# Kernel optimization log

Hardware: AMD Instinct MI355X
Metric: run time of the kernel (lower is better)

## Reference

```python
import jax, jax.numpy as jnp
import numpy as np

H, D = 4, 32            # heads, per-head dim
HD = H * D              # hidden_dim = output_dim = 128
ND, NG = 10000, 30000   # num disease / gene nodes
E_DG, E_GD, E_GG = 150000, 150000, 300000
L = 2                   # num HGTConv layers


def setup_inputs() -> dict:
    key = jax.random.key(0)
    ks = jax.random.split(key, 16)
    s = 0.05
    return {
        "x_d": jax.random.normal(ks[0], (ND, HD), jnp.float32),
        "x_g": jax.random.normal(ks[1], (NG, HD), jnp.float32),
        "src_dg": jax.random.randint(ks[2], (E_DG,), 0, ND),
        "dst_dg": jax.random.randint(ks[3], (E_DG,), 0, NG),
        "src_gd": jax.random.randint(ks[4], (E_GD,), 0, NG),
        "dst_gd": jax.random.randint(ks[5], (E_GD,), 0, ND),
        "src_gg": jax.random.randint(ks[6], (E_GG,), 0, NG),
        "dst_gg": jax.random.randint(ks[7], (E_GG,), 0, NG),
        # fused K/Q/V projection per node type, stacked over layers
        "Wkqv_d": jax.random.normal(ks[8], (L, HD, 3 * HD), jnp.float32) * s,
        "bkqv_d": jnp.zeros((L, 3 * HD), jnp.float32),
        "Wkqv_g": jax.random.normal(ks[9], (L, HD, 3 * HD), jnp.float32) * s,
        "bkqv_g": jnp.zeros((L, 3 * HD), jnp.float32),
        # output linear per node type
        "Wout_d": jax.random.normal(ks[10], (L, HD, HD), jnp.float32) * s,
        "bout_d": jnp.zeros((L, HD), jnp.float32),
        "Wout_g": jax.random.normal(ks[11], (L, HD, HD), jnp.float32) * s,
        "bout_g": jnp.zeros((L, HD), jnp.float32),
        # learnable skip gates per node type
        "skip_d": jnp.ones((L,), jnp.float32),
        "skip_g": jnp.ones((L,), jnp.float32),
        # per edge-type relation matrices (key, message) and priors, 3 edge types
        "arel": jax.random.normal(ks[12], (L, 3, H, D, D), jnp.float32) * s,
        "mrel": jax.random.normal(ks[13], (L, 3, H, D, D), jnp.float32) * s,
        "prel": jnp.ones((L, 3, H), jnp.float32),
    }


def _hgt_forward(x_d, x_g, src_dg, dst_dg, src_gd, dst_gd, src_gg, dst_gg,
                 Wkqv_d, bkqv_d, Wkqv_g, bkqv_g, Wout_d, bout_d, Wout_g, bout_g,
                 skip_d, skip_g, arel, mrel, prel):
    scale = 1.0 / (D ** 0.5)
    for l in range(L):
        def kqv(x, W, b):
            t = (x @ W + b).reshape(-1, 3, H, D)
            return t[:, 0], t[:, 1], t[:, 2]

        k_d, q_d, v_d = kqv(x_d, Wkqv_d[l], bkqv_d[l])
        k_g, q_g, v_g = kqv(x_g, Wkqv_g[l], bkqv_g[l])

        def edge_msgs(k_src, v_src, q_dst, src, dst, et):
            # gather src K/V, transform by per-edge-type relation matrices
            ke = jnp.einsum('ehd,hdf->ehf', k_src[src], arel[l, et])  # [E,H,D]
            ve = jnp.einsum('ehd,hdf->ehf', v_src[src], mrel[l, et])  # [E,H,D]
            a = jnp.sum(q_dst[dst] * ke, axis=-1) * prel[l, et] * scale  # [E,H]
            return a, ve

        a_dg, v_dg = edge_msgs(k_d, v_d, q_g, src_dg, dst_dg, 0)
        a_gd, v_gd = edge_msgs(k_g, v_g, q_d, src_gd, dst_gd, 1)
        a_gg, v_gg = edge_msgs(k_g, v_g, q_g, src_gg, dst_gg, 2)

        def aggregate(alphas, vals, dsts, n):
            # segment softmax over ALL incoming edges of a dst node (across edge types)
            a = jnp.concatenate(alphas, axis=0)
            v = jnp.concatenate(vals, axis=0)
            d = jnp.concatenate(dsts, axis=0)
            amax = jax.ops.segment_max(a, d, num_segments=n)
            ex = jnp.exp(a - amax[d])
            den = jax.ops.segment_sum(ex, d, num_segments=n)
            w = ex / den[d]
            out = jax.ops.segment_sum(w[:, :, None] * v, d, num_segments=n)
            return out.reshape(n, HD)

        agg_g = aggregate([a_dg, a_gg], [v_dg, v_gg], [dst_dg, dst_gg], NG)
        agg_d = aggregate([a_gd], [v_gd], [dst_gd], ND)

        def update(agg, x, Wout, bout, skip):
            o = jax.nn.gelu(agg) @ Wout + bout
            g = jax.nn.sigmoid(skip)
            return g * o + (1.0 - g) * x

        x_d = update(agg_d, x_d, Wout_d[l], bout_d[l], skip_d[l])
        x_g = update(agg_g, x_g, Wout_g[l], bout_g[l], skip_g[l])
    return x_d, x_g


def reference(x_d, x_g, src_dg, dst_dg, src_gd, dst_gd, src_gg, dst_gg,
              Wkqv_d, bkqv_d, Wkqv_g, bkqv_g, Wout_d, bout_d, Wout_g, bout_g,
              skip_d, skip_g, arel, mrel, prel):
    return _hgt_forward(x_d, x_g, src_dg, dst_dg, src_gd, dst_gd, src_gg, dst_gg,
                        Wkqv_d, bkqv_d, Wkqv_g, bkqv_g, Wout_d, bout_d, Wout_g, bout_g,
                        skip_d, skip_g, arel, mrel, prel)
```

## Files before the change

kernel.cpp:

```cpp
#include <hip/hip_runtime.h>
#include <hip/hip_bf16.h>

#define H 4
#define D 32
#define HD 128
#define ND 10000
#define NG 30000
#define E_DG 150000
#define E_GD 150000
#define E_GG 300000
#define NE (E_DG + E_GD + E_GG)
#define EG (E_DG + E_GG)
#define NLAYER 2
#define NBG 30
#define NBD 10
#define NSCAN (NBG + NBD)
#define OCG 640
#define OCD 384
#define GOFF ((size_t)ND * OCD)
#define NSCAT 2344
#define NQUAD 625
#define XLSTRIDE 136

typedef _Float16 f16;
typedef __attribute__((ext_vector_type(2))) _Float16 f16x2;
typedef __attribute__((ext_vector_type(4))) _Float16 f16x4;
typedef __attribute__((ext_vector_type(8))) _Float16 f16x8;
typedef __attribute__((ext_vector_type(4))) float f32x4;

__device__ __forceinline__ float bu(unsigned short u) {
    return __uint_as_float(((unsigned)u) << 16);
}
__device__ __forceinline__ float ldraw(const void* p, size_t i, bool isf32) {
    return isf32 ? ((const float*)p)[i] : bu(((const unsigned short*)p)[i]);
}
__device__ __forceinline__ float gelu(float v) {
    const float c = 0.79788456080286536f * (v + 0.044715f * v * v * v);
    return 0.5f * v * (1.0f + tanhf(c));
}

__device__ __forceinline__ void combine_one(
    int idx, int GENE, bool isf32,
    const void* W, const void* bvec,
    const void* arel, const void* mrel, const void* prel,
    f16* __restrict__ Wp, float* __restrict__ bp) {
    const int OC = GENE ? OCG : OCD;
    const int l = idx / (OC * 128);
    const int rem = idx - l * OC * 128;
    const int col = rem >> 7;
    const int d = rem & 127;
    const int g = col >> 7;
    const int jj = col & 127;
    const int h = jj >> 5, f = jj & 31;
    const size_t wbase = (size_t)l * 128 * 384;
    const size_t bbase = (size_t)l * 384;
    float val, bv = 0.f;
    if (g == 0) {
        val = ldraw(W, wbase + d * 384 + 128 + jj, isf32);
        bv = ldraw(bvec, bbase + 128 + jj, isf32);
    } else {
        const int et = GENE ? ((g <= 2) ? 1 : 2) : 0;
        const bool isk = (g & 1);
        const void* mat = isk ? arel : mrel;
        const size_t mbase = (((size_t)(l * 3 + et) * H + h) << 10) + f;
        const int sb = isk ? 0 : 256;
        val = 0.f;
        for (int dd = 0; dd < 32; dd++)
            val += ldraw(W, wbase + d * 384 + sb + h * 32 + dd, isf32) *
                   ldraw(mat, mbase + dd * 32, isf32);
        if (d == 0)
            for (int dd = 0; dd < 32; dd++)
                bv += ldraw(bvec, bbase + sb + h * 32 + dd, isf32) *
                      ldraw(mat, mbase + dd * 32, isf32);
        if (isk) {
            const float sc = ldraw(prel, (size_t)(l * 3 + et) * H + h, isf32) *
                             (0.17677669529663689f * 1.4426950408889634f);
            val *= sc;
            bv *= sc;
        }
    }
    Wp[(size_t)l * 4 * OC * 32 + ((size_t)(d >> 5) * OC + col) * 32 + (d & 31)] = (f16)val;
    if (d == 0) bp[l * OC + col] = bv;
}

__global__ __launch_bounds__(256) void k_prep0(
    const void* x0,
    const void* wkqvd_r, const void* bkqvd_r,
    const void* wkqvg_r, const void* bkqvg_r,
    const void* arel_r, const void* mrel_r, const void* prel_r,
    const void* woutd_r, const void* woutg_r,
    const void* boutd_r, const void* boutg_r,
    const void* skipd_r, const void* skipg_r,
    f16* __restrict__ Wp_d, float* __restrict__ bp_d,
    f16* __restrict__ Wp_g, float* __restrict__ bp_g,
    f16* __restrict__ Wpod, f16* __restrict__ Wpog,
    float* __restrict__ boutc_d, float* __restrict__ boutc_g,
    float* __restrict__ gates, int* __restrict__ flag,
    const int* __restrict__ dst_dg, const int* __restrict__ dst_gg,
    const int* __restrict__ dst_gd,
    int* __restrict__ cnt_g, int* __restrict__ cnt_d,
    int* __restrict__ rank, int* __restrict__ ready) {
    const int tid = threadIdx.x;
    const int b = blockIdx.x;
    if (b >= 1281) {
        const int i = (b - 1281) * 256 + tid;
        if (i < E_DG) rank[i] = atomicAdd(cnt_g + dst_dg[i], 1);
        else if (i < EG) rank[i] = atomicAdd(cnt_g + dst_gg[i - E_DG], 1);
        else if (i < NE) rank[i] = atomicAdd(cnt_d + dst_gd[i - EG], 1);
        return;
    }
    __shared__ int sbad;
    if (tid == 0) sbad = 0;
    __syncthreads();
    {
        const unsigned short* xs = (const unsigned short*)x0;
        int bad = 0;
        for (int i = tid; i < 1024; i += 256)
            if (!(fabsf(bu(xs[i])) < 1e6f)) bad = 1;
        if (bad) sbad = 1;
    }
    __syncthreads();
    const bool isf32 = (sbad != 0);

    if (b < 1280) {
        int idx = b * 256 + tid;
        const int nd = NLAYER * OCD * 128;
        const int ng = NLAYER * OCG * 128;
        const int np = 2 * NLAYER * 128 * 128;
        if (idx < nd) {
            combine_one(idx, 0, isf32, wkqvd_r, bkqvd_r, arel_r, mrel_r, prel_r, Wp_d, bp_d);
        } else if ((idx -= nd) < ng) {
            combine_one(idx, 1, isf32, wkqvg_r, bkqvg_r, arel_r, mrel_r, prel_r, Wp_g, bp_g);
        } else if ((idx -= ng) < np) {
            const int type = idx >= NLAYER * 128 * 128;
            int rem = idx - type * NLAYER * 128 * 128;
            const int l = rem / (128 * 128);
            rem -= l * 128 * 128;
            const int d = rem >> 7, col = rem & 127;
            const float w = ldraw(type ? woutg_r : woutd_r,
                                  (size_t)l * 128 * 128 + d * 128 + col, isf32);
            f16* out = (type ? Wpog : Wpod) +
                ((size_t)l * 4 + (d >> 5)) * 128 * 32 + col * 32 + (d & 31);
            *out = (f16)w;
        }
    } else {
        if (tid < NSCAN) ready[tid] = 0;
        if (tid == 0) {
            flag[0] = isf32 ? 1 : 0;
            gates[0] = 1.f / (1.f + expf(-ldraw(skipd_r, 0, isf32)));
            gates[1] = 1.f / (1.f + expf(-ldraw(skipg_r, 0, isf32)));
            gates[2] = 1.f / (1.f + expf(-ldraw(skipd_r, 1, isf32)));
            gates[3] = 1.f / (1.f + expf(-ldraw(skipg_r, 1, isf32)));
        }
        for (int i = tid; i < NLAYER * 128; i += 256) {
            boutc_d[i] = ldraw(boutd_r, i, isf32);
            boutc_g[i] = ldraw(boutg_r, i, isf32);
        }
    }
}

__device__ __forceinline__ void kqv_block_4mt(
    const f16* xls, int tid, int mt0,
    const f16* __restrict__ Wpd, const float* __restrict__ bpd,
    const f16* __restrict__ Wpg, const float* __restrict__ bpg,
    f16* __restrict__ tab) {
    const int wv = tid >> 6, lane = tid & 63;
    const int r = lane & 15, q4 = lane >> 4;
    const bool g0 = (mt0 * 16 >= ND);
    const bool g3 = ((mt0 + 3) * 16 >= ND);
    if (g0 == g3) {
        const bool gene = g0;
        const int OC = gene ? OCG : OCD;
        const f16* Wp = gene ? Wpg : Wpd;
        const float* bias = gene ? bpg : bpd;
        f16* out = gene ? (tab + GOFF) : tab;
        const int trow0 = mt0 * 16 - (gene ? ND : 0);
        const int nt = gene ? 10 : 6;
        for (int ntl = wv; ntl < nt; ntl += 4) {
            const int col0 = ntl << 6;
            f16x8 B[4][4];
#pragma unroll
            for (int kb = 0; kb < 4; kb++) {
                const f16* wb = Wp + ((size_t)kb * OC + col0 + r) * 32 + q4 * 8;
#pragma unroll
                for (int t = 0; t < 4; t++) B[kb][t] = *(const f16x8*)(wb + t * 512);
            }
#pragma unroll 1
            for (int mtl = 0; mtl < 4; mtl++) {
                f32x4 acc[4];
                acc[0] = acc[1] = acc[2] = acc[3] = (f32x4){0.f, 0.f, 0.f, 0.f};
#pragma unroll
                for (int kb = 0; kb < 4; kb++) {
                    const f16x8 a = *(const f16x8*)(xls + (mtl * 16 + r) * XLSTRIDE + kb * 32 + q4 * 8);
#pragma unroll
                    for (int t = 0; t < 4; t++)
                        acc[t] = __builtin_amdgcn_mfma_f32_16x16x32_f16(B[kb][t], a, acc[t], 0, 0, 0);
                }
#pragma unroll
                for (int t = 0; t < 4; t++) {
                    const int col = col0 + t * 16 + q4 * 4;
                    const f32x4 bb = *(const f32x4*)(bias + col);
                    f16x4 o;
#pragma unroll
                    for (int reg = 0; reg < 4; reg++)
                        o[reg] = (f16)(acc[t][reg] + bb[reg]);
                    *(f16x4*)(out + (size_t)(trow0 + mtl * 16 + r) * OC + col) = o;
                }
            }
        }
    } else {
        for (int mtl = 0; mtl < 4; mtl++) {
            const int node0 = (mt0 + mtl) * 16;
            const bool gene = (node0 >= ND);
            const int OC = gene ? OCG : OCD;
            const f16* Wp = gene ? Wpg : Wpd;
            const float* bias = gene ? bpg : bpd;
            f16* out = gene ? (tab + GOFF) : tab;
            const int trow0 = node0 - (gene ? ND : 0);
            const int nt = gene ? 10 : 6;
            for (int ntl = wv; ntl < nt; ntl += 4) {
                const int col0 = ntl << 6;
                f32x4 acc[4];
                acc[0] = acc[1] = acc[2] = acc[3] = (f32x4){0.f, 0.f, 0.f, 0.f};
#pragma unroll
                for (int kb = 0; kb < 4; kb++) {
                    const f16x8 a = *(const f16x8*)(xls + (mtl * 16 + r) * XLSTRIDE + kb * 32 + q4 * 8);
                    const f16* wb = Wp + ((size_t)kb * OC + col0 + r) * 32 + q4 * 8;
#pragma unroll
                    for (int t = 0; t < 4; t++) {
                        const f16x8 bt = *(const f16x8*)(wb + t * 512);
                        acc[t] = __builtin_amdgcn_mfma_f32_16x16x32_f16(bt, a, acc[t], 0, 0, 0);
                    }
                }
#pragma unroll
                for (int t = 0; t < 4; t++) {
                    const int col = col0 + t * 16 + q4 * 4;
                    const f32x4 bb = *(const f32x4*)(bias + col);
                    f16x4 o;
#pragma unroll
                    for (int reg = 0; reg < 4; reg++)
                        o[reg] = (f16)(acc[t][reg] + bb[reg]);
                    *(f16x4*)(out + (size_t)(trow0 + r) * OC + col) = o;
                }
            }
        }
    }
}

__global__ __launch_bounds__(256) void k_scangemm0(
    const int* __restrict__ cnt_g, const int* __restrict__ cnt_d,
    int* __restrict__ ready,
    int* __restrict__ rp_g, int* __restrict__ rp_d,
    const void* xd_r, const void* xg_r, const int* __restrict__ flag,
    const f16* __restrict__ Wpd, const float* __restrict__ bpd,
    const f16* __restrict__ Wpg, const float* __restrict__ bpg,
    f16* __restrict__ tab) {
    __shared__ int sdata[256];
    __shared__ int red2[256];
    __shared__ int s_off;
    __shared__ f16 xls[64 * XLSTRIDE];
    const int tid = threadIdx.x;
    if (blockIdx.x < NSCAN) {
        const int b = blockIdx.x;
        const bool isg = (b < NBG);
        const int* cnt = isg ? cnt_g : cnt_d;
        int* rp = isg ? rp_g : rp_d;
        const int n = isg ? NG : ND;
        const int lb = isg ? b : (b - NBG);
        const int i0 = lb * 1024 + tid * 4;
        int v[4];
        int t = 0;
#pragma unroll
        for (int j = 0; j < 4; j++) {
            v[j] = (i0 + j < n) ? cnt[i0 + j] : 0;
            t += v[j];
        }
        sdata[tid] = t;
        __syncthreads();
        for (int d = 1; d < 256; d <<= 1) {
            const int u = (tid >= d) ? sdata[tid - d] : 0;
            __syncthreads();
            sdata[tid] += u;
            __syncthreads();
        }
        const int total = sdata[255];
        if (tid == 0) atomicExch(&ready[b], total + 1);
        const int p0 = isg ? 0 : NBG;
        const int npred = b - p0;
        int part = 0;
        for (int i = tid; i < npred; i += 256) {
            int vv;
            do { vv = atomicAdd(&ready[p0 + i], 0); } while (vv == 0);
            part += vv - 1;
        }
        red2[tid] = part;
        __syncthreads();
        for (int d = 128; d > 0; d >>= 1) {
            if (tid < d) red2[tid] += red2[tid + d];
            __syncthreads();
        }
        if (tid == 0) s_off = red2[0];
        __syncthreads();
        int run = s_off + sdata[tid] - t;
#pragma unroll
        for (int j = 0; j < 4; j++) {
            if (i0 + j < n) {
                run += v[j];
                rp[i0 + j + 1] = run;
            }
        }
        if (tid == 0 && lb == 0) rp[0] = 0;
        return;
    }
    const bool isf32 = (*flag != 0);
    const int mt0 = (blockIdx.x - NSCAN) * 4;
    for (int i = tid; i < 2048; i += 256) {
        const int row = i >> 5;
        const int c4 = (i & 31) * 4;
        const int gnode = mt0 * 16 + row;
        const bool gene = (gnode >= ND);
        const void* xr = gene ? xg_r : xd_r;
        const size_t base = (size_t)(gene ? gnode - ND : gnode) * 128 + c4;
        float4 v;
        if (isf32) {
            v = *(const float4*)((const float*)xr + base);
        } else {
            const ushort4 u = *(const ushort4*)((const unsigned short*)xr + base);
            v = make_float4(bu(u.x), bu(u.y), bu(u.z), bu(u.w));
        }
        f16* dst = xls + row * XLSTRIDE + c4;
        dst[0] = (f16)v.x; dst[1] = (f16)v.y; dst[2] = (f16)v.z; dst[3] = (f16)v.w;
    }
    __syncthreads();
    kqv_block_4mt(xls, tid, mt0, Wpd, bpd, Wpg, bpg, tab);
}

__global__ __launch_bounds__(256) void k_scatter(
    const int* __restrict__ src_dg, const int* __restrict__ dst_dg,
    const int* __restrict__ src_gg, const int* __restrict__ dst_gg,
    const int* __restrict__ src_gd, const int* __restrict__ dst_gd,
    const int* __restrict__ rp_g, const int* __restrict__ rp_d,
    const int* __restrict__ rank,
    int* __restrict__ edges_g, int* __restrict__ edges_d) {
    const int i = blockIdx.x * 256 + threadIdx.x;
    if (i < E_DG) {
        edges_g[rp_g[dst_dg[i]] + rank[i]] = src_dg[i] * OCD + 128;
    } else if (i < EG) {
        const int j = i - E_DG;
        edges_g[rp_g[dst_gg[j]] + rank[i]] = (int)GOFF + src_gg[j] * OCG + 384;
    } else if (i < NE) {
        const int j = i - EG;
        edges_d[rp_d[dst_gd[j]] + rank[i]] = (int)GOFF + src_gd[j] * OCG + 128;
    }
}

__global__ __launch_bounds__(256) void k_agg(
    const int* __restrict__ rp_g, const int* __restrict__ edges_g,
    const int* __restrict__ rp_d, const int* __restrict__ edges_d,
    const f16* __restrict__ tab, f16* __restrict__ gagg) {
    const int wid = blockIdx.x * 4 + (threadIdx.x >> 6);
    const int lane = threadIdx.x & 63;
    const int slot = lane >> 4, sub = lane & 15;

    int node, row;
    const int *rp, *edges;
    size_t qoff;
    if (wid < NG) {
        node = wid; rp = rp_g; edges = edges_g;
        qoff = GOFF + (size_t)node * OCG;
        row = ND + node;
    } else {
        node = wid - NG; rp = rp_d; edges = edges_d;
        qoff = (size_t)node * OCD;
        row = node;
    }

    union U { f16x8 v; f16x2 p[4]; };
    U q;
    q.v = *(const f16x8*)(tab + qoff + sub * 8);

    float s = 0.f;
    float acc[8];
#pragma unroll
    for (int i = 0; i < 8; i++) acc[i] = 0.f;

    const int r0 = rp[node], r1 = rp[node + 1];
    int e = r0 + slot;

    auto kvload = [&](int rec, U& k, U& v) {
        const f16* p = tab + (size_t)rec + sub * 8;
        k.v = *(const f16x8*)p;
        v.v = *(const f16x8*)(p + 128);
    };

    int recA0 = (e < r1) ? edges[e] : 0;
    int recB0 = (e + 4 < r1) ? edges[e + 4] : 0;
    U kA0, vA0, kB0, vB0;
    kvload(recA0, kA0, vA0);
    kvload(recB0, kB0, vB0);
    int recA1 = (e + 8 < r1) ? edges[e + 8] : 0;
    int recB1 = (e + 12 < r1) ? edges[e + 12] : 0;

    while (e < r1) {
        const int recA2 = (e + 16 < r1) ? edges[e + 16] : 0;
        const int recB2 = (e + 20 < r1) ? edges[e + 20] : 0;
        U kA1, vA1, kB1, vB1;
        kvload(recA1, kA1, vA1);
        kvload(recB1, kB1, vB1);

        float pA = __builtin_amdgcn_fdot2(q.p[0], kA0.p[0], 0.f, false);
        float pB = __builtin_amdgcn_fdot2(q.p[0], kB0.p[0], 0.f, false);
        pA = __builtin_amdgcn_fdot2(q.p[1], kA0.p[1], pA, false);
        pB = __builtin_amdgcn_fdot2(q.p[1], kB0.p[1], pB, false);
        pA = __builtin_amdgcn_fdot2(q.p[2], kA0.p[2], pA, false);
        pB = __builtin_amdgcn_fdot2(q.p[2], kB0.p[2], pB, false);
        pA = __builtin_amdgcn_fdot2(q.p[3], kA0.p[3], pA, false);
        pB = __builtin_amdgcn_fdot2(q.p[3], kB0.p[3], pB, false);
        pA += __shfl_xor(pA, 1);
        pB += __shfl_xor(pB, 1);
        pA += __shfl_xor(pA, 2);
        pB += __shfl_xor(pB, 2);
        const float eaA = exp2f(pA);
        const float eaB = (e + 4 < r1) ? exp2f(pB) : 0.f;
        s += eaA + eaB;
#pragma unroll
        for (int i = 0; i < 8; i++)
            acc[i] = fmaf(eaB, (float)vB0.v[i], fmaf(eaA, (float)vA0.v[i], acc[i]));
        recA0 = recA1; recB0 = recB1; recA1 = recA2; recB1 = recB2;
        kA0 = kA1; vA0 = vA1; kB0 = kB1; vB0 = vB1;
        e += 8;
    }

#pragma unroll
    for (int mask = 16; mask <= 32; mask <<= 1) {
        s += __shfl_xor(s, mask);
#pragma unroll
        for (int i = 0; i < 8; i++) acc[i] += __shfl_xor(acc[i], mask);
    }

    const float inv = (s > 0.f) ? (1.f / s) : 0.f;
    if (slot == 0) {
        f16x8 o;
#pragma unroll
        for (int i = 0; i < 8; i++) o[i] = (f16)gelu(acc[i] * inv);
        *(f16x8*)(gagg + (size_t)row * HD + sub * 8) = o;
    }
}

__global__ __launch_bounds__(256) void k_updgemm(
    const f16* __restrict__ gagg,
    const f16* __restrict__ Wpod0, const f16* __restrict__ Wpog0,
    const float* __restrict__ boutc_d0, const float* __restrict__ boutc_g0,
    const float* __restrict__ gates,
    const void* xd_r, const void* xg_r, const int* __restrict__ flag,
    f16* __restrict__ xball,
    const f16* __restrict__ Wpd1, const float* __restrict__ bpd1,
    const f16* __restrict__ Wpg1, const float* __restrict__ bpg1,
    f16* __restrict__ tab) {
    __shared__ f16 xls[64 * XLSTRIDE];
    const bool isf32 = (*flag != 0);
    const int tid = threadIdx.x;
    const int wv = tid >> 6, lane = tid & 63;
    const int r = lane & 15, q4 = lane >> 4;

    {
        const int nt = wv & 1, col0 = nt << 6;
        f16x8 B[4][4];
        int prevg = -1;
#pragma unroll 1
        for (int p = 0; p < 2; p++) {
            const int mtl = (wv >> 1) + p * 2;
            const int node0 = (blockIdx.x * 4 + mtl) * 16;
            const bool gene = (node0 >= ND);
            const f16* Wp = gene ? Wpog0 : Wpod0;
            const float* bias = gene ? boutc_g0 : boutc_d0;
            const float g = gates[gene ? 1 : 0];
            if ((int)gene != prevg) {
                prevg = (int)gene;
#pragma unroll
                for (int kb = 0; kb < 4; kb++) {
                    const f16* wb = Wp + ((size_t)kb * 128 + col0 + r) * 32 + q4 * 8;
#pragma unroll
                    for (int t = 0; t < 4; t++) B[kb][t] = *(const f16x8*)(wb + t * 512);
                }
            }
            f32x4 acc[4];
            acc[0] = acc[1] = acc[2] = acc[3] = (f32x4){0.f, 0.f, 0.f, 0.f};
#pragma unroll
            for (int kb = 0; kb < 4; kb++) {
                const f16x8 a = *(const f16x8*)(gagg + (size_t)(node0 + r) * 128 + kb * 32 + q4 * 8);
#pragma unroll
                for (int t = 0; t < 4; t++)
                    acc[t] = __builtin_amdgcn_mfma_f32_16x16x32_f16(B[kb][t], a, acc[t], 0, 0, 0);
            }
            const void* xr = gene ? xg_r : xd_r;
            const int lrow0 = node0 - (gene ? ND : 0);
#pragma unroll
            for (int t = 0; t < 4; t++) {
                const int col = col0 + t * 16 + q4 * 4;
                const f32x4 bb = *(const f32x4*)(bias + col);
                const size_t xbase = (size_t)(lrow0 + r) * 128 + col;
                float xo[4];
                if (isf32) {
                    const f32x4 u = *(const f32x4*)((const float*)xr + xbase);
#pragma unroll
                    for (int reg = 0; reg < 4; reg++) xo[reg] = u[reg];
                } else {
                    const ushort4 u = *(const ushort4*)((const unsigned short*)xr + xbase);
                    xo[0] = bu(u.x); xo[1] = bu(u.y); xo[2] = bu(u.z); xo[3] = bu(u.w);
                }
                f16x4 xv;
#pragma unroll
                for (int reg = 0; reg < 4; reg++) {
                    const float xn = g * (acc[t][reg] + bb[reg]) + (1.f - g) * xo[reg];
                    xv[reg] = (f16)xn;
                }
                *(f16x4*)(xls + (mtl * 16 + r) * XLSTRIDE + col) = xv;
                *(f16x4*)(xball + (size_t)(node0 + r) * 128 + col) = xv;
            }
        }
    }
    __syncthreads();

    kqv_block_4mt(xls, tid, blockIdx.x * 4, Wpd1, bpd1, Wpg1, bpg1, tab);
}

__global__ __launch_bounds__(256) void k_upd1(
    const f16* __restrict__ gagg,
    const f16* __restrict__ Wpod1, const f16* __restrict__ Wpog1,
    const float* __restrict__ boutc_d1, const float* __restrict__ boutc_g1,
    const float* __restrict__ gates,
    const f16* __restrict__ xball, float* __restrict__ dout) {
    const int tid = threadIdx.x;
    const int wv = tid >> 6, lane = tid & 63;
    const int r = lane & 15, q4 = lane >> 4;
    const int nt = wv & 1, col0 = nt << 6;
    f16x8 B[4][4];
    int prevg = -1;
#pragma unroll 1
    for (int p = 0; p < 2; p++) {
        const int mtile = blockIdx.x * 4 + (wv >> 1) * 2 + p;
        const int node0 = mtile * 16;
        const bool gene = (node0 >= ND);
        const f16* Wp = gene ? Wpog1 : Wpod1;
        const float* bias = gene ? boutc_g1 : boutc_d1;
        const float g = gates[gene ? 1 : 0];
        if ((int)gene != prevg) {
            prevg = (int)gene;
#pragma unroll
            for (int kb = 0; kb < 4; kb++) {
                const f16* wb = Wp + ((size_t)kb * 128 + col0 + r) * 32 + q4 * 8;
#pragma unroll
                for (int t = 0; t < 4; t++) B[kb][t] = *(const f16x8*)(wb + t * 512);
            }
        }
        f32x4 acc[4];
        acc[0] = acc[1] = acc[2] = acc[3] = (f32x4){0.f, 0.f, 0.f, 0.f};
#pragma unroll
        for (int kb = 0; kb < 4; kb++) {
            const f16x8 a = *(const f16x8*)(gagg + (size_t)(node0 + r) * 128 + kb * 32 + q4 * 8);
#pragma unroll
            for (int t = 0; t < 4; t++)
                acc[t] = __builtin_amdgcn_mfma_f32_16x16x32_f16(B[kb][t], a, acc[t], 0, 0, 0);
        }
#pragma unroll
        for (int t = 0; t < 4; t++) {
            const int col = col0 + t * 16 + q4 * 4;
            const f32x4 bb = *(const f32x4*)(bias + col);
            const size_t idx = (size_t)(node0 + r) * 128 + col;
            const f16x4 xb = *(const f16x4*)(xball + idx);
            f32x4 o;
#pragma unroll
            for (int reg = 0; reg < 4; reg++)
                o[reg] = g * (acc[t][reg] + bb[reg]) + (1.f - g) * (float)xb[reg];
            *(f32x4*)(dout + idx) = o;
        }
    }
}

static inline size_t alignup(size_t v) { return (v + 15) & ~(size_t)15; }

extern "C" void kernel_launch(void* const* d_in, const int* in_sizes, int n_in,
                              void* d_out, int out_size, void* d_ws, size_t ws_size,
                              hipStream_t stream) {
    (void)in_sizes; (void)n_in; (void)out_size; (void)ws_size;
    const int* src_dg = (const int*)d_in[2];
    const int* dst_dg = (const int*)d_in[3];
    const int* src_gd = (const int*)d_in[4];
    const int* dst_gd = (const int*)d_in[5];
    const int* src_gg = (const int*)d_in[6];
    const int* dst_gg = (const int*)d_in[7];

    float* ws = (float*)d_ws;
    int* flag = (int*)ws; ws += 16;
    int* cnt_g  = (int*)ws; ws += alignup(NG);
    int* cnt_d  = (int*)ws; ws += alignup(ND);
    int* rp_g   = (int*)ws; ws += alignup(NG + 1);
    int* rp_d   = (int*)ws; ws += alignup(ND + 1);
    int* rank   = (int*)ws; ws += alignup(NE);
    int* ready  = (int*)ws; ws += 64;
    int* edges_g = (int*)ws; ws += alignup(EG);
    int* edges_d = (int*)ws; ws += alignup(E_GD);
    float* bp_d = ws; ws += alignup((size_t)NLAYER * OCD);
    float* bp_g = ws; ws += alignup((size_t)NLAYER * OCG);
    float* boutc_d = ws; ws += alignup((size_t)NLAYER * 128);
    float* boutc_g = ws; ws += alignup((size_t)NLAYER * 128);
    float* gates = ws; ws += 16;
    f16* Wp_d = (f16*)ws; ws += alignup((size_t)NLAYER * 4 * OCD * 32 / 2);
    f16* Wp_g = (f16*)ws; ws += alignup((size_t)NLAYER * 4 * OCG * 32 / 2);
    f16* Wpod = (f16*)ws; ws += alignup((size_t)NLAYER * 4 * 128 * 32 / 2);
    f16* Wpog = (f16*)ws; ws += alignup((size_t)NLAYER * 4 * 128 * 32 / 2);
    f16* xball = (f16*)ws; ws += alignup((size_t)(ND + NG) * HD / 2);
    f16* gagg  = (f16*)ws; ws += alignup((size_t)(ND + NG) * HD / 2);
    f16* tab   = (f16*)ws; ws += alignup(((size_t)ND * OCD + (size_t)NG * OCG) / 2);

    hipMemsetAsync(cnt_g, 0, (size_t)(NG + ND) * sizeof(int), stream);
    k_prep0<<<1281 + NSCAT, 256, 0, stream>>>(
        d_in[0],
        d_in[8], d_in[9], d_in[10], d_in[11],
        d_in[18], d_in[19], d_in[20],
        d_in[12], d_in[14], d_in[13], d_in[15], d_in[16], d_in[17],
        Wp_d, bp_d, Wp_g, bp_g, Wpod, Wpog, boutc_d, boutc_g,
        gates, flag,
        dst_dg, dst_gg, dst_gd, cnt_g, cnt_d, rank, ready);
    k_scangemm0<<<NSCAN + NQUAD, 256, 0, stream>>>(
        cnt_g, cnt_d, ready, rp_g, rp_d,
        d_in[0], d_in[1], flag,
        Wp_d, bp_d, Wp_g, bp_g, tab);
    k_scatter<<<NSCAT, 256, 0, stream>>>(
        src_dg, dst_dg, src_gg, dst_gg, src_gd, dst_gd,
        rp_g, rp_d, rank, edges_g, edges_d);
    k_agg<<<(NG + ND) / 4, 256, 0, stream>>>(rp_g, edges_g, rp_d, edges_d, tab, gagg);
    k_updgemm<<<NQUAD, 256, 0, stream>>>(
        gagg, Wpod, Wpog, boutc_d, boutc_g, gates,
        d_in[0], d_in[1], flag, xball,
        Wp_d + (size_t)4 * OCD * 32, bp_d + OCD,
        Wp_g + (size_t)4 * OCG * 32, bp_g + OCG, tab);
    k_agg<<<(NG + ND) / 4, 256, 0, stream>>>(rp_g, edges_g, rp_d, edges_d, tab, gagg);
    k_upd1<<<NQUAD, 256, 0, stream>>>(
        gagg, Wpod + (size_t)4 * 128 * 32, Wpog + (size_t)4 * 128 * 32,
        boutc_d + 128, boutc_g + 128, gates + 2, xball, (float*)d_out);
}
```

Baseline: 305.5 us.

## Fuse edge scatter into scan/GEMM kernel and map one node per 16-lane group

The edge scatter kernel is merged into the scan+KQV GEMM launch as extra blocks. These blocks spin on an atomic counter until all scan blocks have published the row pointers, which removes one kernel launch and lets the scatter overlap the GEMM. The aggregation kernel now gives each 16-lane slot its own destination node instead of splitting one node's edges across four slots. That drops the cross-slot shuffle reduction and launches four times fewer blocks. The trade-offs are that the spin-wait depends on scan blocks being scheduled first, and per-node degree imbalance within a wavefront can cause divergence.

```diff
diff --git a/kernel.cpp b/kernel.cpp
--- a/kernel.cpp
+++ b/kernel.cpp
@@ -145,6 +145,7 @@
         }
     } else {
         if (tid < NSCAN) ready[tid] = 0;
+        if (tid == 63) ready[63] = 0;
         if (tid == 0) {
             flag[0] = isf32 ? 1 : 0;
             gates[0] = 1.f / (1.f + expf(-ldraw(skipd_r, 0, isf32)));
@@ -254,7 +255,12 @@
     const void* xd_r, const void* xg_r, const int* __restrict__ flag,
     const f16* __restrict__ Wpd, const float* __restrict__ bpd,
     const f16* __restrict__ Wpg, const float* __restrict__ bpg,
-    f16* __restrict__ tab) {
+    f16* __restrict__ tab,
+    const int* __restrict__ src_dg, const int* __restrict__ dst_dg,
+    const int* __restrict__ src_gg, const int* __restrict__ dst_gg,
+    const int* __restrict__ src_gd, const int* __restrict__ dst_gd,
+    const int* __restrict__ rank,
+    int* __restrict__ edges_g, int* __restrict__ edges_d) {
     __shared__ int sdata[256];
     __shared__ int red2[256];
     __shared__ int s_off;
@@ -310,39 +316,41 @@
             }
         }
         if (tid == 0 && lb == 0) rp[0] = 0;
+        __threadfence();
+        __syncthreads();
+        if (tid == 0) atomicAdd(&ready[63], 1);
         return;
     }
-    const bool isf32 = (*flag != 0);
-    const int mt0 = (blockIdx.x - NSCAN) * 4;
-    for (int i = tid; i < 2048; i += 256) {
-        const int row = i >> 5;
-        const int c4 = (i & 31) * 4;
-        const int gnode = mt0 * 16 + row;
-        const bool gene = (gnode >= ND);
-        const void* xr = gene ? xg_r : xd_r;
-        const size_t base = (size_t)(gene ? gnode - ND : gnode) * 128 + c4;
-        float4 v;
-        if (isf32) {
-            v = *(const float4*)((const float*)xr + base);
-        } else {
-            const ushort4 u = *(const ushort4*)((const unsigned short*)xr + base);
-            v = make_float4(bu(u.x), bu(u.y), bu(u.z), bu(u.w));
-        }
-        f16* dst = xls + row * XLSTRIDE + c4;
-        dst[0] = (f16)v.x; dst[1] = (f16)v.y; dst[2] = (f16)v.z; dst[3] = (f16)v.w;
+    if (blockIdx.x < NSCAN + NQUAD) {
+        const bool isf32 = (*flag != 0);
+        const int mt0 = (blockIdx.x - NSCAN) * 4;
+        for (int i = tid; i < 2048; i += 256) {
+            const int row = i >> 5;
+            const int c4 = (i & 31) * 4;
+            const int gnode = mt0 * 16 + row;
+            const bool gene = (gnode >= ND);
+            const void* xr = gene ? xg_r : xd_r;
+            const size_t base = (size_t)(gene ? gnode - ND : gnode) * 128 + c4;
+            float4 v;
+            if (isf32) {
+                v = *(const float4*)((const float*)xr + base);
+            } else {
+                const ushort4 u = *(const ushort4*)((const unsigned short*)xr + base);
+                v = make_float4(bu(u.x), bu(u.y), bu(u.z), bu(u.w));
+            }
+            f16* dst = xls + row * XLSTRIDE + c4;
+            dst[0] = (f16)v.x; dst[1] = (f16)v.y; dst[2] = (f16)v.z; dst[3] = (f16)v.w;
+        }
+        __syncthreads();
+        kqv_block_4mt(xls, tid, mt0, Wpd, bpd, Wpg, bpg, tab);
+        return;
+    }
+    if (tid == 0) {
+        while (atomicAdd(&ready[63], 0) < NSCAN) __builtin_amdgcn_s_sleep(8);
     }
     __syncthreads();
-    kqv_block_4mt(xls, tid, mt0, Wpd, bpd, Wpg, bpg, tab);
-}
-
-__global__ __launch_bounds__(256) void k_scatter(
-    const int* __restrict__ src_dg, const int* __restrict__ dst_dg,
-    const int* __restrict__ src_gg, const int* __restrict__ dst_gg,
-    const int* __restrict__ src_gd, const int* __restrict__ dst_gd,
-    const int* __restrict__ rp_g, const int* __restrict__ rp_d,
-    const int* __restrict__ rank,
-    int* __restrict__ edges_g, int* __restrict__ edges_d) {
-    const int i = blockIdx.x * 256 + threadIdx.x;
+    __threadfence();
+    const int i = (blockIdx.x - NSCAN - NQUAD) * 256 + tid;
     if (i < E_DG) {
         edges_g[rp_g[dst_dg[i]] + rank[i]] = src_dg[i] * OCD + 128;
     } else if (i < EG) {
@@ -358,19 +366,19 @@
     const int* __restrict__ rp_g, const int* __restrict__ edges_g,
     const int* __restrict__ rp_d, const int* __restrict__ edges_d,
     const f16* __restrict__ tab, f16* __restrict__ gagg) {
-    const int wid = blockIdx.x * 4 + (threadIdx.x >> 6);
     const int lane = threadIdx.x & 63;
     const int slot = lane >> 4, sub = lane & 15;
+    const int wnode = (blockIdx.x * 4 + (threadIdx.x >> 6)) * 4 + slot;
 
     int node, row;
     const int *rp, *edges;
     size_t qoff;
-    if (wid < NG) {
-        node = wid; rp = rp_g; edges = edges_g;
+    if (wnode < NG) {
+        node = wnode; rp = rp_g; edges = edges_g;
         qoff = GOFF + (size_t)node * OCG;
         row = ND + node;
     } else {
-        node = wid - NG; rp = rp_d; edges = edges_d;
+        node = wnode - NG; rp = rp_d; edges = edges_d;
         qoff = (size_t)node * OCD;
         row = node;
     }
@@ -385,7 +393,7 @@
     for (int i = 0; i < 8; i++) acc[i] = 0.f;
 
     const int r0 = rp[node], r1 = rp[node + 1];
-    int e = r0 + slot;
+    int e = r0;
 
     auto kvload = [&](int rec, U& k, U& v) {
         const f16* p = tab + (size_t)rec + sub * 8;
@@ -393,58 +401,46 @@
         v.v = *(const f16x8*)(p + 128);
     };
 
-    int recA0 = (e < r1) ? edges[e] : 0;
-    int recB0 = (e + 4 < r1) ? edges[e + 4] : 0;
-    U kA0, vA0, kB0, vB0;
-    kvload(recA0, kA0, vA0);
-    kvload(recB0, kB0, vB0);
-    int recA1 = (e + 8 < r1) ? edges[e + 8] : 0;
-    int recB1 = (e + 12 < r1) ? edges[e + 12] : 0;
+    int recA = (e < r1) ? edges[e] : 0;
+    int recB = (e + 1 < r1) ? edges[e + 1] : 0;
+    U kA, vA, kB, vB;
+    kvload(recA, kA, vA);
+    kvload(recB, kB, vB);
 
     while (e < r1) {
-        const int recA2 = (e + 16 < r1) ? edges[e + 16] : 0;
-        const int recB2 = (e + 20 < r1) ? edges[e + 20] : 0;
-        U kA1, vA1, kB1, vB1;
-        kvload(recA1, kA1, vA1);
-        kvload(recB1, kB1, vB1);
-
-        float pA = __builtin_amdgcn_fdot2(q.p[0], kA0.p[0], 0.f, false);
-        float pB = __builtin_amdgcn_fdot2(q.p[0], kB0.p[0], 0.f, false);
-        pA = __builtin_amdgcn_fdot2(q.p[1], kA0.p[1], pA, false);
-        pB = __builtin_amdgcn_fdot2(q.p[1], kB0.p[1], pB, false);
-        pA = __builtin_amdgcn_fdot2(q.p[2], kA0.p[2], pA, false);
-        pB = __builtin_amdgcn_fdot2(q.p[2], kB0.p[2], pB, false);
-        pA = __builtin_amdgcn_fdot2(q.p[3], kA0.p[3], pA, false);
-        pB = __builtin_amdgcn_fdot2(q.p[3], kB0.p[3], pB, false);
+        const int recC = (e + 2 < r1) ? edges[e + 2] : 0;
+        const int recD = (e + 3 < r1) ? edges[e + 3] : 0;
+        U kC, vC, kD, vD;
+        kvload(recC, kC, vC);
+        kvload(recD, kD, vD);
+
+        float pA = __builtin_amdgcn_fdot2(q.p[0], kA.p[0], 0.f, false);
+        float pB = __builtin_amdgcn_fdot2(q.p[0], kB.p[0], 0.f, false);
+        pA = __builtin_amdgcn_fdot2(q.p[1], kA.p[1], pA, false);
+        pB = __builtin_amdgcn_fdot2(q.p[1], kB.p[1], pB, false);
+        pA = __builtin_amdgcn_fdot2(q.p[2], kA.p[2], pA, false);
+        pB = __builtin_amdgcn_fdot2(q.p[2], kB.p[2], pB, false);
+        pA = __builtin_amdgcn_fdot2(q.p[3], kA.p[3], pA, false);
+        pB = __builtin_amdgcn_fdot2(q.p[3], kB.p[3], pB, false);
         pA += __shfl_xor(pA, 1);
         pB += __shfl_xor(pB, 1);
         pA += __shfl_xor(pA, 2);
         pB += __shfl_xor(pB, 2);
         const float eaA = exp2f(pA);
-        const float eaB = (e + 4 < r1) ? exp2f(pB) : 0.f;
+        const float eaB = (e + 1 < r1) ? exp2f(pB) : 0.f;
         s += eaA + eaB;
 #pragma unroll
         for (int i = 0; i < 8; i++)
-            acc[i] = fmaf(eaB, (float)vB0.v[i], fmaf(eaA, (float)vA0.v[i], acc[i]));
-        recA0 = recA1; recB0 = recB1; recA1 = recA2; recB1 = recB2;
-        kA0 = kA1; vA0 = vA1; kB0 = kB1; vB0 = vB1;
-        e += 8;
-    }
-
-#pragma unroll
-    for (int mask = 16; mask <= 32; mask <<= 1) {
-        s += __shfl_xor(s, mask);
-#pragma unroll
-        for (int i = 0; i < 8; i++) acc[i] += __shfl_xor(acc[i], mask);
+            acc[i] = fmaf(eaB, (float)vB.v[i], fmaf(eaA, (float)vA.v[i], acc[i]));
+        kA = kC; vA = vC; kB = kD; vB = vD;
+        e += 2;
     }
 
     const float inv = (s > 0.f) ? (1.f / s) : 0.f;
-    if (slot == 0) {
-        f16x8 o;
-#pragma unroll
-        for (int i = 0; i < 8; i++) o[i] = (f16)gelu(acc[i] * inv);
-        *(f16x8*)(gagg + (size_t)row * HD + sub * 8) = o;
-    }
+    f16x8 o;
+#pragma unroll
+    for (int i = 0; i < 8; i++) o[i] = (f16)gelu(acc[i] * inv);
+    *(f16x8*)(gagg + (size_t)row * HD + sub * 8) = o;
 }
 
 __global__ __launch_bounds__(256) void k_updgemm(
@@ -623,20 +619,19 @@
         Wp_d, bp_d, Wp_g, bp_g, Wpod, Wpog, boutc_d, boutc_g,
         gates, flag,
         dst_dg, dst_gg, dst_gd, cnt_g, cnt_d, rank, ready);
-    k_scangemm0<<<NSCAN + NQUAD, 256, 0, stream>>>(
+    k_scangemm0<<<NSCAN + NQUAD + NSCAT, 256, 0, stream>>>(
         cnt_g, cnt_d, ready, rp_g, rp_d,
         d_in[0], d_in[1], flag,
-        Wp_d, bp_d, Wp_g, bp_g, tab);
-    k_scatter<<<NSCAT, 256, 0, stream>>>(
+        Wp_d, bp_d, Wp_g, bp_g, tab,
         src_dg, dst_dg, src_gg, dst_gg, src_gd, dst_gd,
-        rp_g, rp_d, rank, edges_g, edges_d);
-    k_agg<<<(NG + ND) / 4, 256, 0, stream>>>(rp_g, edges_g, rp_d, edges_d, tab, gagg);
+        rank, edges_g, edges_d);
+    k_agg<<<(NG + ND) / 16, 256, 0, stream>>>(rp_g, edges_g, rp_d, edges_d, tab, gagg);
     k_updgemm<<<NQUAD, 256, 0, stream>>>(
         gagg, Wpod, Wpog, boutc_d, boutc_g, gates,
         d_in[0], d_in[1], flag, xball,
         Wp_d + (size_t)4 * OCD * 32, bp_d + OCD,
         Wp_g + (size_t)4 * OCG * 32, bp_g + OCG, tab);
-    k_agg<<<(NG + ND) / 4, 256, 0, stream>>>(rp_g, edges_g, rp_d, edges_d, tab, gagg);
+    k_agg<<<(NG + ND) / 16, 256, 0, stream>>>(rp_g, edges_g, rp_d, edges_d, tab, gagg);
     k_upd1<<<NQUAD, 256, 0, stream>>>(
         gagg, Wpod + (size_t)4 * 128 * 32, Wpog + (size_t)4 * 128 * 32,
         boutc_d + 128, boutc_g + 128, gates + 2, xball, (float*)d_out);
```

Result: slower. 621.2 us (+103.3%).

## Fuse edge scatter into scan/GEMM kernel via global ready counter; vectorize weight loads

Applied to the files above, without the earlier changes.

Removes the separate k_scatter launch. After the scan blocks finish they bump a global ready counter, and the GEMM blocks spin on it once their KQV tile is done, then scatter edges in a grid-stride loop. This saves one kernel launch and lets the scatter overlap with GEMM tails, but it relies on all scan blocks being scheduled, which is a deadlock risk if GEMM blocks occupy the device first. The relation-weight combine in prep also loads its 32 W values with vector loads instead of scalar strided loads.

```diff
diff --git a/kernel.cpp b/kernel.cpp
--- a/kernel.cpp
+++ b/kernel.cpp
@@ -26,6 +26,7 @@
 typedef __attribute__((ext_vector_type(2))) _Float16 f16x2;
 typedef __attribute__((ext_vector_type(4))) _Float16 f16x4;
 typedef __attribute__((ext_vector_type(8))) _Float16 f16x8;
+typedef __attribute__((ext_vector_type(8))) unsigned short u16x8;
 typedef __attribute__((ext_vector_type(4))) float f32x4;
 
 __device__ __forceinline__ float bu(unsigned short u) {
@@ -64,10 +65,29 @@
         const void* mat = isk ? arel : mrel;
         const size_t mbase = (((size_t)(l * 3 + et) * H + h) << 10) + f;
         const int sb = isk ? 0 : 256;
+        const size_t wrow = wbase + d * 384 + sb + h * 32;
+        float wv[32];
+        if (isf32) {
+            const float* wp = (const float*)W + wrow;
+#pragma unroll
+            for (int j = 0; j < 8; j++) {
+                const f32x4 u = *(const f32x4*)(wp + j * 4);
+#pragma unroll
+                for (int t = 0; t < 4; t++) wv[j * 4 + t] = u[t];
+            }
+        } else {
+            const unsigned short* wp = (const unsigned short*)W + wrow;
+#pragma unroll
+            for (int j = 0; j < 4; j++) {
+                const u16x8 u = *(const u16x8*)(wp + j * 8);
+#pragma unroll
+                for (int t = 0; t < 8; t++) wv[j * 8 + t] = bu(u[t]);
+            }
+        }
         val = 0.f;
+#pragma unroll
         for (int dd = 0; dd < 32; dd++)
-            val += ldraw(W, wbase + d * 384 + sb + h * 32 + dd, isf32) *
-                   ldraw(mat, mbase + dd * 32, isf32);
+            val += wv[dd] * ldraw(mat, mbase + dd * 32, isf32);
         if (d == 0)
             for (int dd = 0; dd < 32; dd++)
                 bv += ldraw(bvec, bbase + sb + h * 32 + dd, isf32) *
@@ -145,6 +165,7 @@
         }
     } else {
         if (tid < NSCAN) ready[tid] = 0;
+        if (tid == 63) ready[63] = 0;
         if (tid == 0) {
             flag[0] = isf32 ? 1 : 0;
             gates[0] = 1.f / (1.f + expf(-ldraw(skipd_r, 0, isf32)));
@@ -254,7 +275,12 @@
     const void* xd_r, const void* xg_r, const int* __restrict__ flag,
     const f16* __restrict__ Wpd, const float* __restrict__ bpd,
     const f16* __restrict__ Wpg, const float* __restrict__ bpg,
-    f16* __restrict__ tab) {
+    f16* __restrict__ tab,
+    const int* __restrict__ src_dg, const int* __restrict__ dst_dg,
+    const int* __restrict__ src_gg, const int* __restrict__ dst_gg,
+    const int* __restrict__ src_gd, const int* __restrict__ dst_gd,
+    const int* __restrict__ rank,
+    int* __restrict__ edges_g, int* __restrict__ edges_d) {
     __shared__ int sdata[256];
     __shared__ int red2[256];
     __shared__ int s_off;
@@ -310,10 +336,14 @@
             }
         }
         if (tid == 0 && lb == 0) rp[0] = 0;
+        __threadfence();
+        __syncthreads();
+        if (tid == 0) atomicAdd(&ready[63], 1);
         return;
     }
     const bool isf32 = (*flag != 0);
-    const int mt0 = (blockIdx.x - NSCAN) * 4;
+    const int gb = blockIdx.x - NSCAN;
+    const int mt0 = gb * 4;
     for (int i = tid; i < 2048; i += 256) {
         const int row = i >> 5;
         const int c4 = (i & 31) * 4;
@@ -333,24 +363,22 @@
     }
     __syncthreads();
     kqv_block_4mt(xls, tid, mt0, Wpd, bpd, Wpg, bpg, tab);
-}
-
-__global__ __launch_bounds__(256) void k_scatter(
-    const int* __restrict__ src_dg, const int* __restrict__ dst_dg,
-    const int* __restrict__ src_gg, const int* __restrict__ dst_gg,
-    const int* __restrict__ src_gd, const int* __restrict__ dst_gd,
-    const int* __restrict__ rp_g, const int* __restrict__ rp_d,
-    const int* __restrict__ rank,
-    int* __restrict__ edges_g, int* __restrict__ edges_d) {
-    const int i = blockIdx.x * 256 + threadIdx.x;
-    if (i < E_DG) {
-        edges_g[rp_g[dst_dg[i]] + rank[i]] = src_dg[i] * OCD + 128;
-    } else if (i < EG) {
-        const int j = i - E_DG;
-        edges_g[rp_g[dst_gg[j]] + rank[i]] = (int)GOFF + src_gg[j] * OCG + 384;
-    } else if (i < NE) {
-        const int j = i - EG;
-        edges_d[rp_d[dst_gd[j]] + rank[i]] = (int)GOFF + src_gd[j] * OCG + 128;
+
+    if (tid == 0) {
+        while (atomicAdd(&ready[63], 0) < NSCAN) __builtin_amdgcn_s_sleep(2);
+    }
+    __syncthreads();
+    __threadfence();
+    for (int i = gb * 256 + tid; i < NE; i += NQUAD * 256) {
+        if (i < E_DG) {
+            edges_g[rp_g[dst_dg[i]] + rank[i]] = src_dg[i] * OCD + 128;
+        } else if (i < EG) {
+            const int j = i - E_DG;
+            edges_g[rp_g[dst_gg[j]] + rank[i]] = (int)GOFF + src_gg[j] * OCG + 384;
+        } else {
+            const int j = i - EG;
+            edges_d[rp_d[dst_gd[j]] + rank[i]] = (int)GOFF + src_gd[j] * OCG + 128;
+        }
     }
 }
 
@@ -626,10 +654,9 @@
     k_scangemm0<<<NSCAN + NQUAD, 256, 0, stream>>>(
         cnt_g, cnt_d, ready, rp_g, rp_d,
         d_in[0], d_in[1], flag,
-        Wp_d, bp_d, Wp_g, bp_g, tab);
-    k_scatter<<<NSCAT, 256, 0, stream>>>(
+        Wp_d, bp_d, Wp_g, bp_g, tab,
         src_dg, dst_dg, src_gg, dst_gg, src_gd, dst_gd,
-        rp_g, rp_d, rank, edges_g, edges_d);
+        rank, edges_g, edges_d);
     k_agg<<<(NG + ND) / 4, 256, 0, stream>>>(rp_g, edges_g, rp_d, edges_d, tab, gagg);
     k_updgemm<<<NQUAD, 256, 0, stream>>>(
         gagg, Wpod, Wpog, boutc_d, boutc_g, gates,
```

Result: slower. 399.4 us (+30.7%).
